# Kernel tuning notes

Hardware: AMD Instinct MI355X
Metric: run time of the kernel (lower is better)

Reference implementation:

```python
import jax, jax.numpy as jnp
import numpy as np

T = 96
CAP_MWH = 800.0
DP_RAMP = 65.0
DT = 0.25
ETA = float(np.sqrt(0.91))
L_MIN = 4
MAX_CHARGE_MWH = 1200.0
P_MAX = 195.0
N = 5 * T  # variable layout: [c, d, yc, yd, soc]
ITERS = 400  # fixed PDHG iterations (stand-in for SCS to eps=1e-5)

_VOFF = {'c': 0, 'd': 1, 'yc': 2, 'yd': 3, 'soc': 4}

def _idx(v, t):
    return _VOFF[v] * T + t

def _build_lp():
    G, h, A, b = [], [], [], []
    def ineq(pairs, rhs):
        r = np.zeros(N)
        for v, t, co in pairs:
            r[_idx(v, t)] += co
        G.append(r); h.append(rhs)
    def eq(pairs, rhs):
        r = np.zeros(N)
        for v, t, co in pairs:
            r[_idx(v, t)] += co
        A.append(r); b.append(rhs)
    for t in range(T):
        ineq([('c', t, 1.0)], P_MAX); ineq([('d', t, 1.0)], P_MAX)
        ineq([('c', t, -1.0)], 0.0); ineq([('d', t, -1.0)], 0.0)
        ineq([('yc', t, -1.0)], 0.0); ineq([('yc', t, 1.0)], 1.0)
        ineq([('yd', t, -1.0)], 0.0); ineq([('yd', t, 1.0)], 1.0)
        ineq([('soc', t, -1.0)], 0.0); ineq([('soc', t, 1.0)], CAP_MWH)
        ineq([('yc', t, 1.0), ('yd', t, 1.0)], 1.0)
        ineq([('c', t, 1.0), ('yc', t, -P_MAX)], 0.0)
        ineq([('d', t, 1.0), ('yd', t, -P_MAX)], 0.0)
    for t in range(1, T):
        ineq([('c', t, 1.0), ('c', t - 1, -1.0)], DP_RAMP)
        ineq([('c', t - 1, 1.0), ('c', t, -1.0)], DP_RAMP)
        ineq([('d', t, 1.0), ('d', t - 1, -1.0)], DP_RAMP)
        ineq([('d', t - 1, 1.0), ('d', t, -1.0)], DP_RAMP)
    for t in range(T - 1):
        ineq([('yc', t, 1.0), ('yd', t + 1, 1.0)], 1.0)
        ineq([('yd', t, 1.0), ('yc', t + 1, 1.0)], 1.0)
    for v in ('yc', 'yd'):
        for t in range(T):
            for k in range(1, L_MIN):
                if t + k >= T:
                    break
                if t > 0:
                    ineq([(v, t + k, -1.0), (v, t, 1.0), (v, t - 1, -1.0)], 0.0)
                else:
                    ineq([(v, t + k, -1.0), (v, t, 1.0)], 0.0)
    ineq([('c', t, DT) for t in range(T)], MAX_CHARGE_MWH)
    eq([('soc', 0, 1.0), ('c', 0, -ETA * DT), ('d', 0, DT / ETA)], 0.0)
    for t in range(1, T):
        eq([('soc', t, 1.0), ('soc', t - 1, -1.0), ('c', t, -ETA * DT), ('d', t, DT / ETA)], 0.0)
    eq([('soc', T - 1, 1.0)], 0.0)
    return np.array(G), np.array(h), np.array(A), np.array(b)

_G, _h, _A, _b = _build_lp()
_M_EQ = _A.shape[0]
_K_np = np.vstack([_A, _G]).astype(np.float32)
_kb_np = np.concatenate([_b, _h]).astype(np.float32)
_LNORM = float(np.linalg.norm(_K_np.astype(np.float64), 2))
TAU = np.float32(0.9 / _LNORM)
SIG = np.float32(0.9 / _LNORM)
K_MAT = jnp.asarray(_K_np)     # (M, N)
KB = jnp.asarray(_kb_np)       # (M,)


def _solve_one(price):
    # LP: min q^T x  s.t.  A x = b, G x <= h   (max price.(d-c)*DT)
    q = DT * jnp.concatenate([price, -price, jnp.zeros(3 * T, price.dtype)])
    def step(carry, _):
        x, y = carry
        x_new = x - TAU * (q + K_MAT.T @ y)
        x_bar = 2.0 * x_new - x
        y_new = y + SIG * (K_MAT @ x_bar - KB)
        # dual cone projection: equality duals free, inequality duals >= 0
        y_new = jnp.concatenate([y_new[:_M_EQ], jnp.maximum(y_new[_M_EQ:], 0.0)])
        return (x_new, y_new), None
    x0 = jnp.zeros(N, price.dtype)
    y0 = jnp.zeros(K_MAT.shape[0], price.dtype)
    (x, _), _ = jax.lax.scan(step, (x0, y0), None, length=ITERS)
    return x[:T], x[T:2 * T]  # (c, d)


def setup_inputs() -> dict:
    key = jax.random.key(0)
    # realistic-ish electricity prices: ~N(400, 100) CNY/MWh
    price = 400.0 + 100.0 * jax.random.normal(key, (256, T), dtype=jnp.float32)
    return {"price_pred": price}


def reference(price_pred):
    c, d = jax.vmap(_solve_one)(price_pred)  # each (B, 96)
    return c, d
```

## Files before the change

kernel.cpp:

```cpp
#include <hip/hip_runtime.h>
#include <math.h>


#define NITER 400
#define PITER 10

typedef float v2 __attribute__((ext_vector_type(2)));

__device__ __forceinline__ float dpp_shr1(float x) {
  return __int_as_float(__builtin_amdgcn_update_dpp(
      0, __float_as_int(x), 0x138, 0xf, 0xf, true));
}
__device__ __forceinline__ float dpp_shl1(float x) {
  return __int_as_float(__builtin_amdgcn_update_dpp(
      0, __float_as_int(x), 0x130, 0xf, 0xf, true));
}

__device__ __forceinline__ float wave_sum64(float v) {
  float r = v;
  int x;
  x = __builtin_amdgcn_update_dpp(0, __float_as_int(r), 0x111, 0xf, 0xf, true);
  r += __int_as_float(x);
  x = __builtin_amdgcn_update_dpp(0, __float_as_int(r), 0x112, 0xf, 0xf, true);
  r += __int_as_float(x);
  x = __builtin_amdgcn_update_dpp(0, __float_as_int(r), 0x114, 0xf, 0xf, true);
  r += __int_as_float(x);
  x = __builtin_amdgcn_update_dpp(0, __float_as_int(r), 0x118, 0xf, 0xf, true);
  r += __int_as_float(x);
  x = __builtin_amdgcn_update_dpp(0, __float_as_int(r), 0x142, 0xa, 0xf, true);
  r += __int_as_float(x);
  x = __builtin_amdgcn_update_dpp(0, __float_as_int(r), 0x143, 0xc, 0xf, true);
  r += __int_as_float(x);
  return __int_as_float(__builtin_amdgcn_readlane(__float_as_int(r), 63));
}

__global__ __launch_bounds__(64, 1)
void lp_solve_kernel(const float* __restrict__ price, float* __restrict__ out) {
  const int lane = threadIdx.x;
  const int bi = blockIdx.x;
  const double ETA_D = sqrt(0.91);
  const float cET = (float)(-(ETA_D * 0.25));
  const float cDE = (float)(0.25 / ETA_D);
  const v2 Z = {0.f, 0.f};

  const float act = (lane < 48) ? 1.f : 0.f;
  const v2 m_r  = { (lane >= 1 && lane < 48) ? 1.f : 0.f, act };
  const v2 m_sw = { act, (lane <= 46) ? 1.f : 0.f };
  const v2 m_md[3] = {
    { act,                      (lane <= 46) ? 1.f : 0.f },
    { (lane <= 46) ? 1.f : 0.f, (lane <= 46) ? 1.f : 0.f },
    { (lane <= 46) ? 1.f : 0.f, (lane <= 45) ? 1.f : 0.f }
  };

  v2 xc = Z, xd = Z, xyc = Z, xyd = Z, xs = Z;
  v2 xbc = Z, xbd = Z, xbyc = Z, xbyd = Z, xbs = Z;
  v2 qc = Z, qd = Z;
  v2 yb[13];
#pragma unroll
  for (int i = 0; i < 13; ++i) yb[i] = Z;
  v2 ymc[3] = {Z, Z, Z}, ymd[3] = {Z, Z, Z};
  v2 yr[4] = {Z, Z, Z, Z};
  v2 sw0 = Z, sw1 = Z, yeq = Z;
  float yeq96 = 0.f, ytc = 0.f;
  v2 uc = Z, ud = Z, msc = Z, msd = Z;

  float sigv = 0.f, tauv = 0.f;
  float sa = 0.f;
  v2 sr = Z, ssw = Z, smd[3] = {Z, Z, Z};

  auto phaseB = [&](bool power) {
    v2 pxc  = { dpp_shr1(xbc.y),  xbc.x };
    v2 pxd  = { dpp_shr1(xbd.y),  xbd.x };
    v2 pxs  = { dpp_shr1(xbs.y),  xbs.x };
    v2 pxyc = { dpp_shr1(xbyc.y), xbyc.x };
    v2 pxyd = { dpp_shr1(xbyd.y), xbyd.x };
    float a1 = dpp_shl1(xbyc.x), b1 = dpp_shl1(xbyc.y), c1 = dpp_shl1(a1);
    v2 nyc1 = { xbyc.y, a1 };
    v2 nyc2 = { a1, b1 };
    v2 nyc3 = { b1, c1 };
    float a2 = dpp_shl1(xbyd.x), b2 = dpp_shl1(xbyd.y), c2 = dpp_shl1(a2);
    v2 nyd1 = { xbyd.y, a2 };
    v2 nyd2 = { a2, b2 };
    v2 nyd3 = { b2, c2 };

    const v2 c_ = xbc, d_ = xbd, yc_ = xbyc, yd_ = xbyd, s_ = xbs;
    if (power) {
      yb[0] = c_;   yb[1] = d_;
      yb[2] = -c_;  yb[3] = -d_;
      yb[4] = -yc_; yb[5] = yc_;
      yb[6] = -yd_; yb[7] = yd_;
      yb[8] = -s_;  yb[9] = s_;
      yb[10] = yc_ + yd_;
      yb[11] = c_ - 195.f * yc_;
      yb[12] = d_ - 195.f * yd_;
    } else {
      yb[0]  = __builtin_elementwise_max(yb[0]  + sa * (c_ - 195.f), Z);
      yb[1]  = __builtin_elementwise_max(yb[1]  + sa * (d_ - 195.f), Z);
      yb[2]  = __builtin_elementwise_max(yb[2]  - sa * c_,           Z);
      yb[3]  = __builtin_elementwise_max(yb[3]  - sa * d_,           Z);
      yb[4]  = __builtin_elementwise_max(yb[4]  - sa * yc_,          Z);
      yb[5]  = __builtin_elementwise_max(yb[5]  + sa * (yc_ - 1.f),  Z);
      yb[6]  = __builtin_elementwise_max(yb[6]  - sa * yd_,          Z);
      yb[7]  = __builtin_elementwise_max(yb[7]  + sa * (yd_ - 1.f),  Z);
      yb[8]  = __builtin_elementwise_max(yb[8]  - sa * s_,           Z);
      yb[9]  = __builtin_elementwise_max(yb[9]  + sa * (s_ - 800.f), Z);
      yb[10] = __builtin_elementwise_max(yb[10] + sa * (yc_ + yd_ - 1.f), Z);
      yb[11] = __builtin_elementwise_max(yb[11] + sa * (c_ - 195.f * yc_), Z);
      yb[12] = __builtin_elementwise_max(yb[12] + sa * (d_ - 195.f * yd_), Z);
    }
    {
      v2 base_c = yc_ - pxyc, base_d = yd_ - pxyd;
      v2 dc1 = base_c - nyc1, dc2 = base_c - nyc2, dc3 = base_c - nyc3;
      v2 dd1 = base_d - nyd1, dd2 = base_d - nyd2, dd3 = base_d - nyd3;
      if (power) {
        ymc[0] = m_md[0] * dc1; ymc[1] = m_md[1] * dc2; ymc[2] = m_md[2] * dc3;
        ymd[0] = m_md[0] * dd1; ymd[1] = m_md[1] * dd2; ymd[2] = m_md[2] * dd3;
      } else {
        ymc[0] = __builtin_elementwise_max(ymc[0] + smd[0] * dc1, Z);
        ymc[1] = __builtin_elementwise_max(ymc[1] + smd[1] * dc2, Z);
        ymc[2] = __builtin_elementwise_max(ymc[2] + smd[2] * dc3, Z);
        ymd[0] = __builtin_elementwise_max(ymd[0] + smd[0] * dd1, Z);
        ymd[1] = __builtin_elementwise_max(ymd[1] + smd[1] * dd2, Z);
        ymd[2] = __builtin_elementwise_max(ymd[2] + smd[2] * dd3, Z);
      }
    }
    {
      v2 dc = c_ - pxc, dd = d_ - pxd;
      if (power) {
        yr[0] = m_r * dc; yr[1] = -m_r * dc;
        yr[2] = m_r * dd; yr[3] = -m_r * dd;
      } else {
        yr[0] = __builtin_elementwise_max(yr[0] + sr * (dc - 65.f),  Z);
        yr[1] = __builtin_elementwise_max(yr[1] + sr * (-dc - 65.f), Z);
        yr[2] = __builtin_elementwise_max(yr[2] + sr * (dd - 65.f),  Z);
        yr[3] = __builtin_elementwise_max(yr[3] + sr * (-dd - 65.f), Z);
      }
    }
    {
      v2 d0 = yc_ + nyd1, d1 = yd_ + nyc1;
      if (power) { sw0 = m_sw * d0; sw1 = m_sw * d1; }
      else {
        sw0 = __builtin_elementwise_max(sw0 + ssw * (d0 - 1.f), Z);
        sw1 = __builtin_elementwise_max(sw1 + ssw * (d1 - 1.f), Z);
      }
    }
    {
      v2 de = s_ - pxs + cET * c_ + cDE * d_;
      if (power) yeq = act * de;
      else yeq += sa * de;
    }
    uc = yr[0] - yr[1];
    ud = yr[2] - yr[3];
    msc = ymc[0] + ymc[1] + ymc[2];
    msd = ymd[0] + ymd[1] + ymd[2];
    {
      float s95 = __int_as_float(__builtin_amdgcn_readlane(__float_as_int(xbs.y), 47));
      if (power) yeq96 = s95; else yeq96 += sigv * s95;
      float tot = wave_sum64(xbc.x + xbc.y);
      if (power) ytc = 0.25f * tot;
      else ytc = fmaxf(ytc + sigv * (0.25f * tot - 1200.f), 0.f);
    }
  };

  v2 gc, gd, gyc, gyd, gs;
  auto gather = [&]() {
    v2 ucn  = { uc.y,  dpp_shl1(uc.x) };
    v2 udn  = { ud.y,  dpp_shl1(ud.x) };
    v2 mscn = { msc.y, dpp_shl1(msc.x) };
    v2 msdn = { msd.y, dpp_shl1(msd.x) };
    float tdn = dpp_shl1(yeq.x);
    v2 eqn = { yeq.y, (lane == 47) ? -yeq96 : tdn };
    v2 sw1p = { dpp_shr1(sw1.y), sw1.x };
    v2 sw0p = { dpp_shr1(sw0.y), sw0.x };
    v2 pc1 = { dpp_shr1(ymc[0].y), ymc[0].x };
    v2 pc2 = { dpp_shr1(ymc[1].x), dpp_shr1(ymc[1].y) };
    v2 pc3 = { dpp_shr1(dpp_shr1(ymc[2].y)), dpp_shr1(ymc[2].x) };
    v2 pd1 = { dpp_shr1(ymd[0].y), ymd[0].x };
    v2 pd2 = { dpp_shr1(ymd[1].x), dpp_shr1(ymd[1].y) };
    v2 pd3 = { dpp_shr1(dpp_shr1(ymd[2].y)), dpp_shr1(ymd[2].x) };
    gc = (yb[0] - yb[2] + yb[11]) + uc - ucn + 0.25f * ytc + cET * yeq;
    gd = (yb[1] - yb[3] + yb[12]) + ud - udn + cDE * yeq;
    gyc = (-yb[4] + yb[5] + yb[10] - 195.f * yb[11])
        + sw0 + sw1p + msc - mscn - pc1 - pc2 - pc3;
    gyd = (-yb[6] + yb[7] + yb[10] - 195.f * yb[12])
        + sw1 + sw0p + msd - msdn - pd1 - pd2 - pd3;
    gs = (-yb[8] + yb[9]) + yeq - eqn;
  };

  xbc = act; xbd = act; xbyc = act; xbyd = act; xbs = act;
  float lam2 = 1.f;
  for (int pit = 0; pit < PITER; ++pit) {
    phaseB(true);
    gather();
    v2 pv = gc * gc + gd * gd + gyc * gyc + gyd * gyd + gs * gs;
    float part = (pv.x + pv.y) * act;
    lam2 = sqrtf(wave_sum64(part));
    float inv = act / lam2;
    xbc = gc * inv; xbd = gd * inv;
    xbyc = gyc * inv; xbyd = gyd * inv; xbs = gs * inv;
  }
  tauv = (float)(0.9 / sqrt((double)lam2));
  sigv = tauv;
  sa = sigv * act;
  sr = sigv * m_r;
  ssw = sigv * m_sw;
#pragma unroll
  for (int k = 0; k < 3; ++k) smd[k] = sigv * m_md[k];

#pragma unroll
  for (int i = 0; i < 13; ++i) yb[i] = Z;
#pragma unroll
  for (int k = 0; k < 3; ++k) { ymc[k] = Z; ymd[k] = Z; }
#pragma unroll
  for (int k = 0; k < 4; ++k) yr[k] = Z;
  sw0 = Z; sw1 = Z; yeq = Z;
  uc = Z; ud = Z; msc = Z; msd = Z;
  xbc = Z; xbd = Z; xbyc = Z; xbyd = Z; xbs = Z;
  xc = Z; xd = Z; xyc = Z; xyd = Z; xs = Z;
  yeq96 = 0.f; ytc = 0.f;

  {
    const int l2 = (lane < 48) ? lane : 0;
    float p0 = price[bi * 96 + 2 * l2];
    float p1 = price[bi * 96 + 2 * l2 + 1];
    qc = (v2){ 0.25f * p0, 0.25f * p1 };
    qd = (v2){ -0.25f * p0, -0.25f * p1 };
  }

  const float ta = tauv * act;
#pragma unroll 1
  for (int it = 0; it < NITER; ++it) {
    gather();
    {
      v2 xa;
      xa = xc  - ta * (qc + gc);  xbc  = 2.f * xa - xc;  xc  = xa;
      xa = xd  - ta * (qd + gd);  xbd  = 2.f * xa - xd;  xd  = xa;
      xa = xyc - ta * gyc;        xbyc = 2.f * xa - xyc; xyc = xa;
      xa = xyd - ta * gyd;        xbyd = 2.f * xa - xyd; xyd = xa;
      xa = xs  - ta * gs;         xbs  = 2.f * xa - xs;  xs  = xa;
    }
    phaseB(false);
  }

  if (lane < 48) {
    out[bi * 96 + 2 * lane]             = xc.x;
    out[bi * 96 + 2 * lane + 1]         = xc.y;
    out[24576 + bi * 96 + 2 * lane]     = xd.x;
    out[24576 + bi * 96 + 2 * lane + 1] = xd.y;
  }
}

extern "C" void kernel_launch(void* const* d_in, const int* in_sizes, int n_in,
                              void* d_out, int out_size, void* d_ws, size_t ws_size,
                              hipStream_t stream) {
  const float* price = (const float*)d_in[0];
  float* outp = (float*)d_out;
  hipLaunchKernelGGL(lp_solve_kernel, dim3(256), dim3(64), 0, stream, price, outp);
}
```

Before: 225.6 us.

## Split each LP solve across two wavefronts with shared-memory halo exchange

Each problem's 96 time steps move from one wave holding two steps per lane to two waves of 64 threads, each lane holding one step, with overlapping halo lanes. Boundary values of the extrapolated primal and the per-wave partial charge sums are swapped through shared memory behind a __syncthreads every iteration, double-buffered by iteration parity. This halves the per-lane serial arithmetic of each PDHG step and so shortens the dependent chain. In exchange it adds a block barrier, LDS traffic and redundant halo work in every one of the 400 iterations.

Result: slower. 331.6 us (+47.0%).

```diff
diff --git a/kernel.cpp b/kernel.cpp
--- a/kernel.cpp
+++ b/kernel.cpp
@@ -4,8 +4,6 @@
 
 #define NITER 400
 #define PITER 10
-
-typedef float v2 __attribute__((ext_vector_type(2)));
 
 __device__ __forceinline__ float dpp_shr1(float x) {
   return __int_as_float(__builtin_amdgcn_update_dpp(
@@ -34,219 +32,203 @@
   return __int_as_float(__builtin_amdgcn_readlane(__float_as_int(r), 63));
 }
 
-__global__ __launch_bounds__(64, 1)
+__global__ __launch_bounds__(128, 1)
 void lp_solve_kernel(const float* __restrict__ price, float* __restrict__ out) {
-  const int lane = threadIdx.x;
-  const int bi = blockIdx.x;
+  __shared__ float ex[70];
+
+  const int tid = threadIdx.x, lane = tid & 63, wid = tid >> 6, bi = blockIdx.x;
   const double ETA_D = sqrt(0.91);
   const float cET = (float)(-(ETA_D * 0.25));
   const float cDE = (float)(0.25 / ETA_D);
-  const v2 Z = {0.f, 0.f};
-
-  const float act = (lane < 48) ? 1.f : 0.f;
-  const v2 m_r  = { (lane >= 1 && lane < 48) ? 1.f : 0.f, act };
-  const v2 m_sw = { act, (lane <= 46) ? 1.f : 0.f };
-  const v2 m_md[3] = {
-    { act,                      (lane <= 46) ? 1.f : 0.f },
-    { (lane <= 46) ? 1.f : 0.f, (lane <= 46) ? 1.f : 0.f },
-    { (lane <= 46) ? 1.f : 0.f, (lane <= 45) ? 1.f : 0.f }
+
+  const int t = wid ? (lane + 44) : lane;
+  const bool ownB = wid ? (lane >= 4 && lane <= 51) : (lane <= 47);
+  const float own = ownB ? 1.f : 0.f;
+  const float dact = (wid ? (lane >= 1 && lane <= 51) : (lane <= 48)) ? 1.f : 0.f;
+  const float m_r  = (wid ? (lane >= 1 && lane <= 51) : (lane >= 1 && lane <= 48)) ? 1.f : 0.f;
+  const float m_sw = (wid ? (lane >= 1 && lane <= 50) : (lane <= 48)) ? 1.f : 0.f;
+  const float m_m1 = (wid ? (lane >= 1 && lane <= 50) : (lane <= 48)) ? 1.f : 0.f;
+  const float m_m2 = (wid ? (lane >= 1 && lane <= 49) : (lane <= 48)) ? 1.f : 0.f;
+  const float m_m3 = (wid ? (lane >= 1 && lane <= 48) : (lane <= 48)) ? 1.f : 0.f;
+  const bool isL95 = (wid == 1 && lane == 51);
+
+  float xc = 0, xd = 0, xyc = 0, xyd = 0, xs = 0;
+  float xbc = 0, xbd = 0, xbyc = 0, xbyd = 0, xbs = 0;
+  float qc = 0, qd = 0;
+  float yb0=0,yb1=0,yb2=0,yb3=0,yb4=0,yb5=0,yb6=0,yb7=0,yb8=0,yb9=0,yb10=0,yb11=0,yb12=0;
+  float ymc0=0, ymc1=0, ymc2=0, ymd0=0, ymd1=0, ymd2=0;
+  float yr0=0, yr1=0, yr2=0, yr3=0, sw0=0, sw1=0, yeq=0;
+  float uc=0, ud=0, msc=0, msd=0;
+  float ytc = 0.f, yeq96 = 0.f;
+  float sigv = 0.f, tauv = 0.f;
+  float sa=0, sr=0, ssw=0, sm1=0, sm2=0, sm3=0, ta=0;
+
+  auto phaseB = [&](bool power) {
+    float pxc = dpp_shr1(xbc), pxd = dpp_shr1(xbd), pxs = dpp_shr1(xbs);
+    float pxyc = dpp_shr1(xbyc), pxyd = dpp_shr1(xbyd);
+    float nyc1 = dpp_shl1(xbyc), nyc2 = dpp_shl1(nyc1), nyc3 = dpp_shl1(nyc2);
+    float nyd1 = dpp_shl1(xbyd), nyd2 = dpp_shl1(nyd1), nyd3 = dpp_shl1(nyd2);
+    float bc = xbyc - pxyc, bd = xbyd - pxyd;
+    float dc = xbc - pxc, dd = xbd - pxd;
+    if (power) {
+      yb0 = xbc;   yb1 = xbd;
+      yb2 = -xbc;  yb3 = -xbd;
+      yb4 = -xbyc; yb5 = xbyc;
+      yb6 = -xbyd; yb7 = xbyd;
+      yb8 = -xbs;  yb9 = xbs;
+      yb10 = xbyc + xbyd;
+      yb11 = xbc - 195.f * xbyc;
+      yb12 = xbd - 195.f * xbyd;
+      ymc0 = m_m1 * (bc - nyc1); ymc1 = m_m2 * (bc - nyc2); ymc2 = m_m3 * (bc - nyc3);
+      ymd0 = m_m1 * (bd - nyd1); ymd1 = m_m2 * (bd - nyd2); ymd2 = m_m3 * (bd - nyd3);
+      yr0 = m_r * dc; yr1 = -m_r * dc; yr2 = m_r * dd; yr3 = -m_r * dd;
+      sw0 = m_sw * (xbyc + nyd1); sw1 = m_sw * (xbyd + nyc1);
+      yeq = dact * (xbs - pxs + cET * xbc + cDE * xbd);
+      yeq96 = __int_as_float(__builtin_amdgcn_readlane(__float_as_int(xbs), 51));
+    } else {
+      yb0  = fmaxf(yb0  + sa * (xbc - 195.f), 0.f);
+      yb1  = fmaxf(yb1  + sa * (xbd - 195.f), 0.f);
+      yb2  = fmaxf(yb2  - sa * xbc,           0.f);
+      yb3  = fmaxf(yb3  - sa * xbd,           0.f);
+      yb4  = fmaxf(yb4  - sa * xbyc,          0.f);
+      yb5  = fmaxf(yb5  + sa * (xbyc - 1.f),  0.f);
+      yb6  = fmaxf(yb6  - sa * xbyd,          0.f);
+      yb7  = fmaxf(yb7  + sa * (xbyd - 1.f),  0.f);
+      yb8  = fmaxf(yb8  - sa * xbs,           0.f);
+      yb9  = fmaxf(yb9  + sa * (xbs - 800.f), 0.f);
+      yb10 = fmaxf(yb10 + sa * (xbyc + xbyd - 1.f), 0.f);
+      yb11 = fmaxf(yb11 + sa * (xbc - 195.f * xbyc), 0.f);
+      yb12 = fmaxf(yb12 + sa * (xbd - 195.f * xbyd), 0.f);
+      ymc0 = fmaxf(ymc0 + sm1 * (bc - nyc1), 0.f);
+      ymc1 = fmaxf(ymc1 + sm2 * (bc - nyc2), 0.f);
+      ymc2 = fmaxf(ymc2 + sm3 * (bc - nyc3), 0.f);
+      ymd0 = fmaxf(ymd0 + sm1 * (bd - nyd1), 0.f);
+      ymd1 = fmaxf(ymd1 + sm2 * (bd - nyd2), 0.f);
+      ymd2 = fmaxf(ymd2 + sm3 * (bd - nyd3), 0.f);
+      yr0 = fmaxf(yr0 + sr * (dc - 65.f),  0.f);
+      yr1 = fmaxf(yr1 + sr * (-dc - 65.f), 0.f);
+      yr2 = fmaxf(yr2 + sr * (dd - 65.f),  0.f);
+      yr3 = fmaxf(yr3 + sr * (-dd - 65.f), 0.f);
+      sw0 = fmaxf(sw0 + ssw * (xbyc + nyd1 - 1.f), 0.f);
+      sw1 = fmaxf(sw1 + ssw * (xbyd + nyc1 - 1.f), 0.f);
+      yeq += sa * (xbs - pxs + cET * xbc + cDE * xbd);
+      float s95 = __int_as_float(__builtin_amdgcn_readlane(__float_as_int(xbs), 51));
+      yeq96 += sigv * s95;
+    }
+    uc = yr0 - yr1; ud = yr2 - yr3;
+    msc = ymc0 + ymc1 + ymc2; msd = ymd0 + ymd1 + ymd2;
   };
 
-  v2 xc = Z, xd = Z, xyc = Z, xyd = Z, xs = Z;
-  v2 xbc = Z, xbd = Z, xbyc = Z, xbyd = Z, xbs = Z;
-  v2 qc = Z, qd = Z;
-  v2 yb[13];
-#pragma unroll
-  for (int i = 0; i < 13; ++i) yb[i] = Z;
-  v2 ymc[3] = {Z, Z, Z}, ymd[3] = {Z, Z, Z};
-  v2 yr[4] = {Z, Z, Z, Z};
-  v2 sw0 = Z, sw1 = Z, yeq = Z;
-  float yeq96 = 0.f, ytc = 0.f;
-  v2 uc = Z, ud = Z, msc = Z, msd = Z;
-
-  float sigv = 0.f, tauv = 0.f;
-  float sa = 0.f;
-  v2 sr = Z, ssw = Z, smd[3] = {Z, Z, Z};
-
-  auto phaseB = [&](bool power) {
-    v2 pxc  = { dpp_shr1(xbc.y),  xbc.x };
-    v2 pxd  = { dpp_shr1(xbd.y),  xbd.x };
-    v2 pxs  = { dpp_shr1(xbs.y),  xbs.x };
-    v2 pxyc = { dpp_shr1(xbyc.y), xbyc.x };
-    v2 pxyd = { dpp_shr1(xbyd.y), xbyd.x };
-    float a1 = dpp_shl1(xbyc.x), b1 = dpp_shl1(xbyc.y), c1 = dpp_shl1(a1);
-    v2 nyc1 = { xbyc.y, a1 };
-    v2 nyc2 = { a1, b1 };
-    v2 nyc3 = { b1, c1 };
-    float a2 = dpp_shl1(xbyd.x), b2 = dpp_shl1(xbyd.y), c2 = dpp_shl1(a2);
-    v2 nyd1 = { xbyd.y, a2 };
-    v2 nyd2 = { a2, b2 };
-    v2 nyd3 = { b2, c2 };
-
-    const v2 c_ = xbc, d_ = xbd, yc_ = xbyc, yd_ = xbyd, s_ = xbs;
-    if (power) {
-      yb[0] = c_;   yb[1] = d_;
-      yb[2] = -c_;  yb[3] = -d_;
-      yb[4] = -yc_; yb[5] = yc_;
-      yb[6] = -yd_; yb[7] = yd_;
-      yb[8] = -s_;  yb[9] = s_;
-      yb[10] = yc_ + yd_;
-      yb[11] = c_ - 195.f * yc_;
-      yb[12] = d_ - 195.f * yd_;
+  float gc, gd, gyc, gyd, gs;
+  auto gather = [&]() {
+    float ucn = dpp_shl1(uc), udn = dpp_shl1(ud);
+    float mscn = dpp_shl1(msc), msdn = dpp_shl1(msd);
+    float eqn = dpp_shl1(yeq);
+    eqn = isL95 ? -yeq96 : eqn;
+    float sw1p = dpp_shr1(sw1), sw0p = dpp_shr1(sw0);
+    float pc1 = dpp_shr1(ymc0);
+    float a1 = dpp_shr1(ymc1); float pc2 = dpp_shr1(a1);
+    float a2 = dpp_shr1(ymc2); float a3 = dpp_shr1(a2); float pc3 = dpp_shr1(a3);
+    float b1 = dpp_shr1(ymd0); float pd1 = b1;
+    float b2 = dpp_shr1(ymd1); float pd2 = dpp_shr1(b2);
+    float b3 = dpp_shr1(ymd2); float b4 = dpp_shr1(b3); float pd3 = dpp_shr1(b4);
+    gc = (yb0 - yb2 + yb11) + uc - ucn + 0.25f * ytc + cET * yeq;
+    gd = (yb1 - yb3 + yb12) + ud - udn + cDE * yeq;
+    gyc = (yb5 - yb4 + yb10 - 195.f * yb11)
+        + sw0 + sw1p + msc - mscn - pc1 - pc2 - pc3;
+    gyd = (yb7 - yb6 + yb10 - 195.f * yb12)
+        + sw1 + sw0p + msd - msdn - pd1 - pd2 - pd3;
+    gs = (yb9 - yb8) + yeq - eqn;
+  };
+
+  auto exchange = [&](int B, float part) -> float {
+    if (wid == 0) {
+      if (lane >= 44 && lane < 48) {
+        int i = lane - 44;
+        ex[B + i] = xbc; ex[B + 4 + i] = xbd; ex[B + 8 + i] = xbs;
+        ex[B + 12 + i] = xbyc; ex[B + 16 + i] = xbyd;
+      }
     } else {
-      yb[0]  = __builtin_elementwise_max(yb[0]  + sa * (c_ - 195.f), Z);
-      yb[1]  = __builtin_elementwise_max(yb[1]  + sa * (d_ - 195.f), Z);
-      yb[2]  = __builtin_elementwise_max(yb[2]  - sa * c_,           Z);
-      yb[3]  = __builtin_elementwise_max(yb[3]  - sa * d_,           Z);
-      yb[4]  = __builtin_elementwise_max(yb[4]  - sa * yc_,          Z);
-      yb[5]  = __builtin_elementwise_max(yb[5]  + sa * (yc_ - 1.f),  Z);
-      yb[6]  = __builtin_elementwise_max(yb[6]  - sa * yd_,          Z);
-      yb[7]  = __builtin_elementwise_max(yb[7]  + sa * (yd_ - 1.f),  Z);
-      yb[8]  = __builtin_elementwise_max(yb[8]  - sa * s_,           Z);
-      yb[9]  = __builtin_elementwise_max(yb[9]  + sa * (s_ - 800.f), Z);
-      yb[10] = __builtin_elementwise_max(yb[10] + sa * (yc_ + yd_ - 1.f), Z);
-      yb[11] = __builtin_elementwise_max(yb[11] + sa * (c_ - 195.f * yc_), Z);
-      yb[12] = __builtin_elementwise_max(yb[12] + sa * (d_ - 195.f * yd_), Z);
+      if (lane >= 4 && lane < 8) {
+        int i = lane - 4;
+        ex[B + 20 + i] = xbyc; ex[B + 24 + i] = xbyd;
+      }
+      if (lane == 4) { ex[B + 28] = xbc; ex[B + 29] = xbd; ex[B + 30] = xbs; }
     }
-    {
-      v2 base_c = yc_ - pxyc, base_d = yd_ - pxyd;
-      v2 dc1 = base_c - nyc1, dc2 = base_c - nyc2, dc3 = base_c - nyc3;
-      v2 dd1 = base_d - nyd1, dd2 = base_d - nyd2, dd3 = base_d - nyd3;
-      if (power) {
-        ymc[0] = m_md[0] * dc1; ymc[1] = m_md[1] * dc2; ymc[2] = m_md[2] * dc3;
-        ymd[0] = m_md[0] * dd1; ymd[1] = m_md[1] * dd2; ymd[2] = m_md[2] * dd3;
-      } else {
-        ymc[0] = __builtin_elementwise_max(ymc[0] + smd[0] * dc1, Z);
-        ymc[1] = __builtin_elementwise_max(ymc[1] + smd[1] * dc2, Z);
-        ymc[2] = __builtin_elementwise_max(ymc[2] + smd[2] * dc3, Z);
-        ymd[0] = __builtin_elementwise_max(ymd[0] + smd[0] * dd1, Z);
-        ymd[1] = __builtin_elementwise_max(ymd[1] + smd[1] * dd2, Z);
-        ymd[2] = __builtin_elementwise_max(ymd[2] + smd[2] * dd3, Z);
+    if (lane == 0) ex[B + 31 + wid] = part;
+    __syncthreads();
+    if (wid == 0) {
+      if (lane >= 48 && lane < 52) {
+        int i = lane - 48;
+        xbyc = ex[B + 20 + i]; xbyd = ex[B + 24 + i];
+      }
+      if (lane == 48) { xbc = ex[B + 28]; xbd = ex[B + 29]; xbs = ex[B + 30]; }
+    } else {
+      if (lane < 4) {
+        xbc = ex[B + lane]; xbd = ex[B + 4 + lane]; xbs = ex[B + 8 + lane];
+        xbyc = ex[B + 12 + lane]; xbyd = ex[B + 16 + lane];
       }
     }
-    {
-      v2 dc = c_ - pxc, dd = d_ - pxd;
-      if (power) {
-        yr[0] = m_r * dc; yr[1] = -m_r * dc;
-        yr[2] = m_r * dd; yr[3] = -m_r * dd;
-      } else {
-        yr[0] = __builtin_elementwise_max(yr[0] + sr * (dc - 65.f),  Z);
-        yr[1] = __builtin_elementwise_max(yr[1] + sr * (-dc - 65.f), Z);
-        yr[2] = __builtin_elementwise_max(yr[2] + sr * (dd - 65.f),  Z);
-        yr[3] = __builtin_elementwise_max(yr[3] + sr * (-dd - 65.f), Z);
-      }
-    }
-    {
-      v2 d0 = yc_ + nyd1, d1 = yd_ + nyc1;
-      if (power) { sw0 = m_sw * d0; sw1 = m_sw * d1; }
-      else {
-        sw0 = __builtin_elementwise_max(sw0 + ssw * (d0 - 1.f), Z);
-        sw1 = __builtin_elementwise_max(sw1 + ssw * (d1 - 1.f), Z);
-      }
-    }
-    {
-      v2 de = s_ - pxs + cET * c_ + cDE * d_;
-      if (power) yeq = act * de;
-      else yeq += sa * de;
-    }
-    uc = yr[0] - yr[1];
-    ud = yr[2] - yr[3];
-    msc = ymc[0] + ymc[1] + ymc[2];
-    msd = ymd[0] + ymd[1] + ymd[2];
-    {
-      float s95 = __int_as_float(__builtin_amdgcn_readlane(__float_as_int(xbs.y), 47));
-      if (power) yeq96 = s95; else yeq96 += sigv * s95;
-      float tot = wave_sum64(xbc.x + xbc.y);
-      if (power) ytc = 0.25f * tot;
-      else ytc = fmaxf(ytc + sigv * (0.25f * tot - 1200.f), 0.f);
-    }
+    return ex[B + 31] + ex[B + 32];
   };
 
-  v2 gc, gd, gyc, gyd, gs;
-  auto gather = [&]() {
-    v2 ucn  = { uc.y,  dpp_shl1(uc.x) };
-    v2 udn  = { ud.y,  dpp_shl1(ud.x) };
-    v2 mscn = { msc.y, dpp_shl1(msc.x) };
-    v2 msdn = { msd.y, dpp_shl1(msd.x) };
-    float tdn = dpp_shl1(yeq.x);
-    v2 eqn = { yeq.y, (lane == 47) ? -yeq96 : tdn };
-    v2 sw1p = { dpp_shr1(sw1.y), sw1.x };
-    v2 sw0p = { dpp_shr1(sw0.y), sw0.x };
-    v2 pc1 = { dpp_shr1(ymc[0].y), ymc[0].x };
-    v2 pc2 = { dpp_shr1(ymc[1].x), dpp_shr1(ymc[1].y) };
-    v2 pc3 = { dpp_shr1(dpp_shr1(ymc[2].y)), dpp_shr1(ymc[2].x) };
-    v2 pd1 = { dpp_shr1(ymd[0].y), ymd[0].x };
-    v2 pd2 = { dpp_shr1(ymd[1].x), dpp_shr1(ymd[1].y) };
-    v2 pd3 = { dpp_shr1(dpp_shr1(ymd[2].y)), dpp_shr1(ymd[2].x) };
-    gc = (yb[0] - yb[2] + yb[11]) + uc - ucn + 0.25f * ytc + cET * yeq;
-    gd = (yb[1] - yb[3] + yb[12]) + ud - udn + cDE * yeq;
-    gyc = (-yb[4] + yb[5] + yb[10] - 195.f * yb[11])
-        + sw0 + sw1p + msc - mscn - pc1 - pc2 - pc3;
-    gyd = (-yb[6] + yb[7] + yb[10] - 195.f * yb[12])
-        + sw1 + sw0p + msd - msdn - pd1 - pd2 - pd3;
-    gs = (-yb[8] + yb[9]) + yeq - eqn;
-  };
-
-  xbc = act; xbd = act; xbyc = act; xbyd = act; xbs = act;
+  {
+    float vinit = (lane <= 51) ? 1.f : 0.f;
+    xbc = vinit; xbd = vinit; xbyc = vinit; xbyd = vinit; xbs = vinit;
+  }
+  ytc = 0.25f * 96.f;
   float lam2 = 1.f;
   for (int pit = 0; pit < PITER; ++pit) {
     phaseB(true);
     gather();
-    v2 pv = gc * gc + gd * gd + gyc * gyc + gyd * gyd + gs * gs;
-    float part = (pv.x + pv.y) * act;
-    lam2 = sqrtf(wave_sum64(part));
-    float inv = act / lam2;
-    xbc = gc * inv; xbd = gd * inv;
-    xbyc = gyc * inv; xbyd = gyd * inv; xbs = gs * inv;
+    float part = wave_sum64(own * (gc * gc + gd * gd + gyc * gyc + gyd * gyd + gs * gs));
+    if (lane == 0) ex[33 + wid] = part;
+    __syncthreads();
+    lam2 = sqrtf(ex[33] + ex[34]);
+    float inv = own / lam2;
+    xbc = gc * inv; xbd = gd * inv; xbyc = gyc * inv; xbyd = gyd * inv; xbs = gs * inv;
+    float pc = wave_sum64(own * xbc);
+    float tot = exchange(0, pc);
+    ytc = 0.25f * tot;
   }
   tauv = (float)(0.9 / sqrt((double)lam2));
   sigv = tauv;
-  sa = sigv * act;
-  sr = sigv * m_r;
-  ssw = sigv * m_sw;
-#pragma unroll
-  for (int k = 0; k < 3; ++k) smd[k] = sigv * m_md[k];
-
-#pragma unroll
-  for (int i = 0; i < 13; ++i) yb[i] = Z;
-#pragma unroll
-  for (int k = 0; k < 3; ++k) { ymc[k] = Z; ymd[k] = Z; }
-#pragma unroll
-  for (int k = 0; k < 4; ++k) yr[k] = Z;
-  sw0 = Z; sw1 = Z; yeq = Z;
-  uc = Z; ud = Z; msc = Z; msd = Z;
-  xbc = Z; xbd = Z; xbyc = Z; xbyd = Z; xbs = Z;
-  xc = Z; xd = Z; xyc = Z; xyd = Z; xs = Z;
-  yeq96 = 0.f; ytc = 0.f;
+  sa = sigv * dact; sr = sigv * m_r; ssw = sigv * m_sw;
+  sm1 = sigv * m_m1; sm2 = sigv * m_m2; sm3 = sigv * m_m3;
+  ta = tauv * own;
+
+  yb0=yb1=yb2=yb3=yb4=yb5=yb6=yb7=yb8=yb9=yb10=yb11=yb12=0.f;
+  ymc0=ymc1=ymc2=ymd0=ymd1=ymd2=0.f;
+  yr0=yr1=yr2=yr3=sw0=sw1=yeq=0.f;
+  uc=ud=msc=msd=0.f;
+  xbc=xbd=xbyc=xbyd=xbs=0.f;
+  xc=xd=xyc=xyd=xs=0.f;
+  ytc = 0.f; yeq96 = 0.f;
 
   {
-    const int l2 = (lane < 48) ? lane : 0;
-    float p0 = price[bi * 96 + 2 * l2];
-    float p1 = price[bi * 96 + 2 * l2 + 1];
-    qc = (v2){ 0.25f * p0, 0.25f * p1 };
-    qd = (v2){ -0.25f * p0, -0.25f * p1 };
-  }
-
-  const float ta = tauv * act;
+    int ti = (t <= 95) ? t : 95;
+    float pr = price[bi * 96 + ti];
+    qc = 0.25f * pr; qd = -0.25f * pr;
+  }
+
 #pragma unroll 1
   for (int it = 0; it < NITER; ++it) {
     gather();
-    {
-      v2 xa;
-      xa = xc  - ta * (qc + gc);  xbc  = 2.f * xa - xc;  xc  = xa;
-      xa = xd  - ta * (qd + gd);  xbd  = 2.f * xa - xd;  xd  = xa;
-      xa = xyc - ta * gyc;        xbyc = 2.f * xa - xyc; xyc = xa;
-      xa = xyd - ta * gyd;        xbyd = 2.f * xa - xyd; xyd = xa;
-      xa = xs  - ta * gs;         xbs  = 2.f * xa - xs;  xs  = xa;
-    }
+    float xa;
+    xa = xc - ta * (qc + gc);  xbc = 2.f * xa - xc;  xc = xa;
+    xa = xd - ta * (qd + gd);  xbd = 2.f * xa - xd;  xd = xa;
+    xa = xyc - ta * gyc;       xbyc = 2.f * xa - xyc; xyc = xa;
+    xa = xyd - ta * gyd;       xbyd = 2.f * xa - xyd; xyd = xa;
+    xa = xs - ta * gs;         xbs = 2.f * xa - xs;  xs = xa;
+    float pc = wave_sum64(own * xbc);
+    float tot = exchange((it & 1) * 35, pc);
+    ytc = fmaxf(ytc + sigv * (0.25f * tot - 1200.f), 0.f);
     phaseB(false);
   }
 
-  if (lane < 48) {
-    out[bi * 96 + 2 * lane]             = xc.x;
-    out[bi * 96 + 2 * lane + 1]         = xc.y;
-    out[24576 + bi * 96 + 2 * lane]     = xd.x;
-    out[24576 + bi * 96 + 2 * lane + 1] = xd.y;
+  if (ownB) {
+    out[bi * 96 + t] = xc;
+    out[24576 + bi * 96 + t] = xd;
   }
 }
 
@@ -255,5 +237,5 @@
                               hipStream_t stream) {
   const float* price = (const float*)d_in[0];
   float* outp = (float*)d_out;
-  hipLaunchKernelGGL(lp_solve_kernel, dim3(256), dim3(64), 0, stream, price, outp);
-}
+  hipLaunchKernelGGL(lp_solve_kernel, dim3(256), dim3(128), 0, stream, price, outp);
+}
```

## Switch per-lane time mapping from interleaved pairs to split halves

Applied to the files above, without the earlier changes.

Each lane now holds timesteps t and t+48 instead of 2t and 2t+1. Neighbour shifts therefore move both components with DPP and fix the seam lane with a readlane and select. Memory accesses become contiguous per half. In exchange, every shift costs two DPP ops plus a readlane and select, where before it cost one DPP and a register swap, so the inner loop likely gains instructions. The masks for the min-duration rows and the boundary handling are rewritten to match.

Measured after the change: 303.0 us. 34.3% more time.

```diff
diff --git a/kernel.cpp b/kernel.cpp
--- a/kernel.cpp
+++ b/kernel.cpp
@@ -14,6 +14,9 @@
 __device__ __forceinline__ float dpp_shl1(float x) {
   return __int_as_float(__builtin_amdgcn_update_dpp(
       0, __float_as_int(x), 0x130, 0xf, 0xf, true));
+}
+__device__ __forceinline__ float rl(float x, int l) {
+  return __int_as_float(__builtin_amdgcn_readlane(__float_as_int(x), l));
 }
 
 __device__ __forceinline__ float wave_sum64(float v) {
@@ -43,14 +46,15 @@
   const float cDE = (float)(0.25 / ETA_D);
   const v2 Z = {0.f, 0.f};
 
-  const float act = (lane < 48) ? 1.f : 0.f;
-  const v2 m_r  = { (lane >= 1 && lane < 48) ? 1.f : 0.f, act };
-  const v2 m_sw = { act, (lane <= 46) ? 1.f : 0.f };
-  const v2 m_md[3] = {
-    { act,                      (lane <= 46) ? 1.f : 0.f },
-    { (lane <= 46) ? 1.f : 0.f, (lane <= 46) ? 1.f : 0.f },
-    { (lane <= 46) ? 1.f : 0.f, (lane <= 45) ? 1.f : 0.f }
-  };
+  const bool actB = (lane < 48);
+  const float av = actB ? 1.f : 0.f;
+  const bool L0 = (lane == 0), L47 = (lane == 47);
+
+  const v2 m_r  = { (lane >= 1 && lane < 48) ? 1.f : 0.f, av };
+  const v2 m_sw = { av, (lane <= 46) ? 1.f : 0.f };
+  const v2 m_m1 = { av, (lane <= 46) ? 1.f : 0.f };
+  const v2 m_m2 = { av, (lane <= 45) ? 1.f : 0.f };
+  const v2 m_m3 = { av, (lane <= 44) ? 1.f : 0.f };
 
   v2 xc = Z, xd = Z, xyc = Z, xyd = Z, xs = Z;
   v2 xbc = Z, xbd = Z, xbyc = Z, xbyd = Z, xbs = Z;
@@ -58,176 +62,146 @@
   v2 yb[13];
 #pragma unroll
   for (int i = 0; i < 13; ++i) yb[i] = Z;
-  v2 ymc[3] = {Z, Z, Z}, ymd[3] = {Z, Z, Z};
-  v2 yr[4] = {Z, Z, Z, Z};
-  v2 sw0 = Z, sw1 = Z, yeq = Z;
+  v2 ymc0 = Z, ymc1 = Z, ymc2 = Z, ymd0 = Z, ymd1 = Z, ymd2 = Z;
+  v2 yr0 = Z, yr1 = Z, yr2 = Z, yr3 = Z, sw0 = Z, sw1 = Z, yeq = Z;
+  v2 uc = Z, ud = Z, msc = Z, msd = Z;
   float yeq96 = 0.f, ytc = 0.f;
-  v2 uc = Z, ud = Z, msc = Z, msd = Z;
-
-  float sigv = 0.f, tauv = 0.f;
-  float sa = 0.f;
-  v2 sr = Z, ssw = Z, smd[3] = {Z, Z, Z};
+  float sigv = 0.f, tauv = 0.f, sa = 0.f;
+  v2 sr = Z, ssw = Z, sm1 = Z, sm2 = Z, sm3 = Z;
+
+  auto prev1 = [&](v2 X) -> v2 {
+    float h = rl(X.x, 47);
+    v2 r;
+    r.x = dpp_shr1(X.x);
+    float ry = dpp_shr1(X.y);
+    r.y = L0 ? h : ry;
+    return r;
+  };
+  auto next1 = [&](v2 X) -> v2 {
+    float h = rl(X.y, 0);
+    v2 r;
+    r.y = dpp_shl1(X.y);
+    float rx = dpp_shl1(X.x);
+    r.x = L47 ? h : rx;
+    return r;
+  };
 
   auto phaseB = [&](bool power) {
-    v2 pxc  = { dpp_shr1(xbc.y),  xbc.x };
-    v2 pxd  = { dpp_shr1(xbd.y),  xbd.x };
-    v2 pxs  = { dpp_shr1(xbs.y),  xbs.x };
-    v2 pxyc = { dpp_shr1(xbyc.y), xbyc.x };
-    v2 pxyd = { dpp_shr1(xbyd.y), xbyd.x };
-    float a1 = dpp_shl1(xbyc.x), b1 = dpp_shl1(xbyc.y), c1 = dpp_shl1(a1);
-    v2 nyc1 = { xbyc.y, a1 };
-    v2 nyc2 = { a1, b1 };
-    v2 nyc3 = { b1, c1 };
-    float a2 = dpp_shl1(xbyd.x), b2 = dpp_shl1(xbyd.y), c2 = dpp_shl1(a2);
-    v2 nyd1 = { xbyd.y, a2 };
-    v2 nyd2 = { a2, b2 };
-    v2 nyd3 = { b2, c2 };
-
-    const v2 c_ = xbc, d_ = xbd, yc_ = xbyc, yd_ = xbyd, s_ = xbs;
+    v2 pxc = prev1(xbc), pxd = prev1(xbd), pxs = prev1(xbs);
+    v2 pxyc = prev1(xbyc), pxyd = prev1(xbyd);
+    v2 nyc1 = next1(xbyc), nyc2 = next1(nyc1), nyc3 = next1(nyc2);
+    v2 nyd1 = next1(xbyd), nyd2 = next1(nyd1), nyd3 = next1(nyd2);
+    v2 bc = xbyc - pxyc, bd = xbyd - pxyd;
+    v2 dc = xbc - pxc, dd = xbd - pxd;
     if (power) {
-      yb[0] = c_;   yb[1] = d_;
-      yb[2] = -c_;  yb[3] = -d_;
-      yb[4] = -yc_; yb[5] = yc_;
-      yb[6] = -yd_; yb[7] = yd_;
-      yb[8] = -s_;  yb[9] = s_;
-      yb[10] = yc_ + yd_;
-      yb[11] = c_ - 195.f * yc_;
-      yb[12] = d_ - 195.f * yd_;
+      yb[0] = xbc;   yb[1] = xbd;
+      yb[2] = -xbc;  yb[3] = -xbd;
+      yb[4] = -xbyc; yb[5] = xbyc;
+      yb[6] = -xbyd; yb[7] = xbyd;
+      yb[8] = -xbs;  yb[9] = xbs;
+      yb[10] = xbyc + xbyd;
+      yb[11] = xbc - 195.f * xbyc;
+      yb[12] = xbd - 195.f * xbyd;
+      ymc0 = m_m1 * (bc - nyc1); ymc1 = m_m2 * (bc - nyc2); ymc2 = m_m3 * (bc - nyc3);
+      ymd0 = m_m1 * (bd - nyd1); ymd1 = m_m2 * (bd - nyd2); ymd2 = m_m3 * (bd - nyd3);
+      yr0 = m_r * dc; yr1 = -yr0; yr2 = m_r * dd; yr3 = -yr2;
+      sw0 = m_sw * (xbyc + nyd1); sw1 = m_sw * (xbyd + nyc1);
+      yeq = av * (xbs - pxs + cET * xbc + cDE * xbd);
+      yeq96 = rl(xbs.y, 47);
     } else {
-      yb[0]  = __builtin_elementwise_max(yb[0]  + sa * (c_ - 195.f), Z);
-      yb[1]  = __builtin_elementwise_max(yb[1]  + sa * (d_ - 195.f), Z);
-      yb[2]  = __builtin_elementwise_max(yb[2]  - sa * c_,           Z);
-      yb[3]  = __builtin_elementwise_max(yb[3]  - sa * d_,           Z);
-      yb[4]  = __builtin_elementwise_max(yb[4]  - sa * yc_,          Z);
-      yb[5]  = __builtin_elementwise_max(yb[5]  + sa * (yc_ - 1.f),  Z);
-      yb[6]  = __builtin_elementwise_max(yb[6]  - sa * yd_,          Z);
-      yb[7]  = __builtin_elementwise_max(yb[7]  + sa * (yd_ - 1.f),  Z);
-      yb[8]  = __builtin_elementwise_max(yb[8]  - sa * s_,           Z);
-      yb[9]  = __builtin_elementwise_max(yb[9]  + sa * (s_ - 800.f), Z);
-      yb[10] = __builtin_elementwise_max(yb[10] + sa * (yc_ + yd_ - 1.f), Z);
-      yb[11] = __builtin_elementwise_max(yb[11] + sa * (c_ - 195.f * yc_), Z);
-      yb[12] = __builtin_elementwise_max(yb[12] + sa * (d_ - 195.f * yd_), Z);
+      yb[0]  = __builtin_elementwise_max(yb[0]  + sa * (xbc - 195.f), Z);
+      yb[1]  = __builtin_elementwise_max(yb[1]  + sa * (xbd - 195.f), Z);
+      yb[2]  = __builtin_elementwise_max(yb[2]  - sa * xbc,           Z);
+      yb[3]  = __builtin_elementwise_max(yb[3]  - sa * xbd,           Z);
+      yb[4]  = __builtin_elementwise_max(yb[4]  - sa * xbyc,          Z);
+      yb[5]  = __builtin_elementwise_max(yb[5]  + sa * (xbyc - 1.f),  Z);
+      yb[6]  = __builtin_elementwise_max(yb[6]  - sa * xbyd,          Z);
+      yb[7]  = __builtin_elementwise_max(yb[7]  + sa * (xbyd - 1.f),  Z);
+      yb[8]  = __builtin_elementwise_max(yb[8]  - sa * xbs,           Z);
+      yb[9]  = __builtin_elementwise_max(yb[9]  + sa * (xbs - 800.f), Z);
+      yb[10] = __builtin_elementwise_max(yb[10] + sa * (xbyc + xbyd - 1.f), Z);
+      yb[11] = __builtin_elementwise_max(yb[11] + sa * (xbc - 195.f * xbyc), Z);
+      yb[12] = __builtin_elementwise_max(yb[12] + sa * (xbd - 195.f * xbyd), Z);
+      ymc0 = __builtin_elementwise_max(ymc0 + sm1 * (bc - nyc1), Z);
+      ymc1 = __builtin_elementwise_max(ymc1 + sm2 * (bc - nyc2), Z);
+      ymc2 = __builtin_elementwise_max(ymc2 + sm3 * (bc - nyc3), Z);
+      ymd0 = __builtin_elementwise_max(ymd0 + sm1 * (bd - nyd1), Z);
+      ymd1 = __builtin_elementwise_max(ymd1 + sm2 * (bd - nyd2), Z);
+      ymd2 = __builtin_elementwise_max(ymd2 + sm3 * (bd - nyd3), Z);
+      yr0 = __builtin_elementwise_max(yr0 + sr * (dc - 65.f),  Z);
+      yr1 = __builtin_elementwise_max(yr1 + sr * (-dc - 65.f), Z);
+      yr2 = __builtin_elementwise_max(yr2 + sr * (dd - 65.f),  Z);
+      yr3 = __builtin_elementwise_max(yr3 + sr * (-dd - 65.f), Z);
+      sw0 = __builtin_elementwise_max(sw0 + ssw * (xbyc + nyd1 - 1.f), Z);
+      sw1 = __builtin_elementwise_max(sw1 + ssw * (xbyd + nyc1 - 1.f), Z);
+      yeq += sa * (xbs - pxs + cET * xbc + cDE * xbd);
+      yeq96 += sigv * rl(xbs.y, 47);
     }
-    {
-      v2 base_c = yc_ - pxyc, base_d = yd_ - pxyd;
-      v2 dc1 = base_c - nyc1, dc2 = base_c - nyc2, dc3 = base_c - nyc3;
-      v2 dd1 = base_d - nyd1, dd2 = base_d - nyd2, dd3 = base_d - nyd3;
-      if (power) {
-        ymc[0] = m_md[0] * dc1; ymc[1] = m_md[1] * dc2; ymc[2] = m_md[2] * dc3;
-        ymd[0] = m_md[0] * dd1; ymd[1] = m_md[1] * dd2; ymd[2] = m_md[2] * dd3;
-      } else {
-        ymc[0] = __builtin_elementwise_max(ymc[0] + smd[0] * dc1, Z);
-        ymc[1] = __builtin_elementwise_max(ymc[1] + smd[1] * dc2, Z);
-        ymc[2] = __builtin_elementwise_max(ymc[2] + smd[2] * dc3, Z);
-        ymd[0] = __builtin_elementwise_max(ymd[0] + smd[0] * dd1, Z);
-        ymd[1] = __builtin_elementwise_max(ymd[1] + smd[1] * dd2, Z);
-        ymd[2] = __builtin_elementwise_max(ymd[2] + smd[2] * dd3, Z);
-      }
-    }
-    {
-      v2 dc = c_ - pxc, dd = d_ - pxd;
-      if (power) {
-        yr[0] = m_r * dc; yr[1] = -m_r * dc;
-        yr[2] = m_r * dd; yr[3] = -m_r * dd;
-      } else {
-        yr[0] = __builtin_elementwise_max(yr[0] + sr * (dc - 65.f),  Z);
-        yr[1] = __builtin_elementwise_max(yr[1] + sr * (-dc - 65.f), Z);
-        yr[2] = __builtin_elementwise_max(yr[2] + sr * (dd - 65.f),  Z);
-        yr[3] = __builtin_elementwise_max(yr[3] + sr * (-dd - 65.f), Z);
-      }
-    }
-    {
-      v2 d0 = yc_ + nyd1, d1 = yd_ + nyc1;
-      if (power) { sw0 = m_sw * d0; sw1 = m_sw * d1; }
-      else {
-        sw0 = __builtin_elementwise_max(sw0 + ssw * (d0 - 1.f), Z);
-        sw1 = __builtin_elementwise_max(sw1 + ssw * (d1 - 1.f), Z);
-      }
-    }
-    {
-      v2 de = s_ - pxs + cET * c_ + cDE * d_;
-      if (power) yeq = act * de;
-      else yeq += sa * de;
-    }
-    uc = yr[0] - yr[1];
-    ud = yr[2] - yr[3];
-    msc = ymc[0] + ymc[1] + ymc[2];
-    msd = ymd[0] + ymd[1] + ymd[2];
-    {
-      float s95 = __int_as_float(__builtin_amdgcn_readlane(__float_as_int(xbs.y), 47));
-      if (power) yeq96 = s95; else yeq96 += sigv * s95;
-      float tot = wave_sum64(xbc.x + xbc.y);
-      if (power) ytc = 0.25f * tot;
-      else ytc = fmaxf(ytc + sigv * (0.25f * tot - 1200.f), 0.f);
-    }
+    uc = yr0 - yr1; ud = yr2 - yr3;
+    msc = ymc0 + ymc1 + ymc2; msd = ymd0 + ymd1 + ymd2;
+    float tot = wave_sum64(xbc.x + xbc.y);
+    if (power) ytc = 0.25f * tot;
+    else ytc = fmaxf(ytc + sigv * (0.25f * tot - 1200.f), 0.f);
   };
 
   v2 gc, gd, gyc, gyd, gs;
   auto gather = [&]() {
-    v2 ucn  = { uc.y,  dpp_shl1(uc.x) };
-    v2 udn  = { ud.y,  dpp_shl1(ud.x) };
-    v2 mscn = { msc.y, dpp_shl1(msc.x) };
-    v2 msdn = { msd.y, dpp_shl1(msd.x) };
-    float tdn = dpp_shl1(yeq.x);
-    v2 eqn = { yeq.y, (lane == 47) ? -yeq96 : tdn };
-    v2 sw1p = { dpp_shr1(sw1.y), sw1.x };
-    v2 sw0p = { dpp_shr1(sw0.y), sw0.x };
-    v2 pc1 = { dpp_shr1(ymc[0].y), ymc[0].x };
-    v2 pc2 = { dpp_shr1(ymc[1].x), dpp_shr1(ymc[1].y) };
-    v2 pc3 = { dpp_shr1(dpp_shr1(ymc[2].y)), dpp_shr1(ymc[2].x) };
-    v2 pd1 = { dpp_shr1(ymd[0].y), ymd[0].x };
-    v2 pd2 = { dpp_shr1(ymd[1].x), dpp_shr1(ymd[1].y) };
-    v2 pd3 = { dpp_shr1(dpp_shr1(ymd[2].y)), dpp_shr1(ymd[2].x) };
+    v2 ucn = next1(uc), udn = next1(ud);
+    v2 mscn = next1(msc), msdn = next1(msd);
+    v2 eqn = next1(yeq);
+    eqn.y = L47 ? -yeq96 : eqn.y;
+    v2 sw1p = prev1(sw1), sw0p = prev1(sw0);
+    v2 pc1 = prev1(ymc0);
+    v2 t1 = prev1(ymc1); v2 pc2 = prev1(t1);
+    v2 t2 = prev1(ymc2); v2 t3 = prev1(t2); v2 pc3 = prev1(t3);
+    v2 pd1 = prev1(ymd0);
+    v2 u1 = prev1(ymd1); v2 pd2 = prev1(u1);
+    v2 u2 = prev1(ymd2); v2 u3 = prev1(u2); v2 pd3 = prev1(u3);
     gc = (yb[0] - yb[2] + yb[11]) + uc - ucn + 0.25f * ytc + cET * yeq;
     gd = (yb[1] - yb[3] + yb[12]) + ud - udn + cDE * yeq;
-    gyc = (-yb[4] + yb[5] + yb[10] - 195.f * yb[11])
+    gyc = (yb[5] - yb[4] + yb[10] - 195.f * yb[11])
         + sw0 + sw1p + msc - mscn - pc1 - pc2 - pc3;
-    gyd = (-yb[6] + yb[7] + yb[10] - 195.f * yb[12])
+    gyd = (yb[7] - yb[6] + yb[10] - 195.f * yb[12])
         + sw1 + sw0p + msd - msdn - pd1 - pd2 - pd3;
-    gs = (-yb[8] + yb[9]) + yeq - eqn;
-  };
-
-  xbc = act; xbd = act; xbyc = act; xbyd = act; xbs = act;
+    gs = (yb[9] - yb[8]) + yeq - eqn;
+  };
+
+  xbc = av; xbd = av; xbyc = av; xbyd = av; xbs = av;
   float lam2 = 1.f;
   for (int pit = 0; pit < PITER; ++pit) {
     phaseB(true);
     gather();
     v2 pv = gc * gc + gd * gd + gyc * gyc + gyd * gyd + gs * gs;
-    float part = (pv.x + pv.y) * act;
+    float part = (pv.x + pv.y) * av;
     lam2 = sqrtf(wave_sum64(part));
-    float inv = act / lam2;
+    float inv = av / lam2;
     xbc = gc * inv; xbd = gd * inv;
     xbyc = gyc * inv; xbyd = gyd * inv; xbs = gs * inv;
   }
   tauv = (float)(0.9 / sqrt((double)lam2));
   sigv = tauv;
-  sa = sigv * act;
-  sr = sigv * m_r;
-  ssw = sigv * m_sw;
-#pragma unroll
-  for (int k = 0; k < 3; ++k) smd[k] = sigv * m_md[k];
+  sa = sigv * av;
+  sr = sigv * m_r; ssw = sigv * m_sw;
+  sm1 = sigv * m_m1; sm2 = sigv * m_m2; sm3 = sigv * m_m3;
 
 #pragma unroll
   for (int i = 0; i < 13; ++i) yb[i] = Z;
-#pragma unroll
-  for (int k = 0; k < 3; ++k) { ymc[k] = Z; ymd[k] = Z; }
-#pragma unroll
-  for (int k = 0; k < 4; ++k) yr[k] = Z;
-  sw0 = Z; sw1 = Z; yeq = Z;
+  ymc0 = Z; ymc1 = Z; ymc2 = Z; ymd0 = Z; ymd1 = Z; ymd2 = Z;
+  yr0 = Z; yr1 = Z; yr2 = Z; yr3 = Z; sw0 = Z; sw1 = Z; yeq = Z;
   uc = Z; ud = Z; msc = Z; msd = Z;
   xbc = Z; xbd = Z; xbyc = Z; xbyd = Z; xbs = Z;
   xc = Z; xd = Z; xyc = Z; xyd = Z; xs = Z;
   yeq96 = 0.f; ytc = 0.f;
 
   {
-    const int l2 = (lane < 48) ? lane : 0;
-    float p0 = price[bi * 96 + 2 * l2];
-    float p1 = price[bi * 96 + 2 * l2 + 1];
+    const int ti = actB ? lane : 0;
+    float p0 = price[bi * 96 + ti];
+    float p1 = price[bi * 96 + 48 + ti];
     qc = (v2){ 0.25f * p0, 0.25f * p1 };
     qd = (v2){ -0.25f * p0, -0.25f * p1 };
   }
 
-  const float ta = tauv * act;
+  const float ta = tauv * av;
 #pragma unroll 1
   for (int it = 0; it < NITER; ++it) {
     gather();
@@ -242,11 +216,11 @@
     phaseB(false);
   }
 
-  if (lane < 48) {
-    out[bi * 96 + 2 * lane]             = xc.x;
-    out[bi * 96 + 2 * lane + 1]         = xc.y;
-    out[24576 + bi * 96 + 2 * lane]     = xd.x;
-    out[24576 + bi * 96 + 2 * lane + 1] = xd.y;
+  if (actB) {
+    out[bi * 96 + lane]              = xc.x;
+    out[bi * 96 + 48 + lane]         = xc.y;
+    out[24576 + bi * 96 + lane]      = xd.x;
+    out[24576 + bi * 96 + 48 + lane] = xd.y;
   }
 }
 
```
